# Kernel tuning notes

Measured on AMD Instinct MI355X. Metric: run time of the kernel, lower is better.

## Reference

```python
import jax, jax.numpy as jnp
import numpy as np

# loss weights / thresholds (match module defaults)
L_RC, L_HU, L_EDGE, L_TEX = 2.0, 1.5, 1.0, 0.8
L_HF, L_SYN, L_IC, L_MID, L_LF = 1.5, 1.0, 0.8, 0.8, 0.6
MIN_BODY, ART_FACTOR, FLAT_TH = 4096, 2.0, 0.03

SOBEL_X = jnp.array([[-1., 0., 1.], [-2., 0., 2.], [-1., 0., 1.]], jnp.float32)
SOBEL_Y = jnp.array([[-1., -2., -1.], [0., 0., 0.], [1., 2., 1.]], jnp.float32)
LAP = jnp.array([[0., 1., 0.], [1., -4., 1.], [0., 1., 0.]], jnp.float32)

def _conv2d(x, k):
    # x: (B,1,H,W), k: (kh,kw), 'same' padding single-channel conv
    kh, kw = k.shape
    return jax.lax.conv_general_dilated(
        x, k[None, None].astype(x.dtype), (1, 1),
        [(kh // 2, kh // 2), (kw // 2, kw // 2)],
        dimension_numbers=('NCHW', 'OIHW', 'NCHW'))

def _gauss_kernel(sigma):
    k = int(6 * sigma + 1)
    if k % 2 == 0:
        k += 1
    c = jnp.arange(k, dtype=jnp.float32) - k // 2
    g = jnp.exp(-0.5 * (c / sigma) ** 2)
    g = g / g.sum()
    return g[:, None] * g[None, :]

def _masked_mean(x, mask):
    cnt = jnp.sum(mask)
    return jnp.sum(jnp.where(mask, x, 0.0)) / jnp.maximum(cnt, 1)

def _masked_l1(a, b, mask):
    cnt = jnp.sum(mask)
    return jnp.sum(jnp.where(mask, jnp.abs(a - b), 0.0)) / jnp.maximum(cnt, 1)

def _masked_quantile(x, mask, q):
    # torch.quantile(x[mask], q) with linear interpolation
    v = jnp.sort(jnp.where(mask, x, jnp.inf).ravel())
    n = jnp.maximum(jnp.sum(mask), 1)
    pos = q * (n - 1).astype(x.dtype)
    lo = jnp.clip(jnp.floor(pos).astype(jnp.int32), 0, v.size - 1)
    hi = jnp.clip(jnp.ceil(pos).astype(jnp.int32), 0, v.size - 1)
    frac = pos - lo.astype(x.dtype)
    return v[lo] * (1.0 - frac) + v[hi] * frac

def setup_inputs() -> dict:
    key = jax.random.key(0)
    ks = jax.random.split(key, 7)
    B, H, W = 16, 768, 768
    return {
        'y_pred': jax.random.uniform(ks[0], (B, 1, 1, H, W), jnp.float32),
        'noise_pred': jax.random.normal(ks[1], (B, 1, 1, H, W), jnp.float32),
        'x_i': jax.random.uniform(ks[2], (B, 1, H, W), jnp.float32),
        'x_ip1': jax.random.uniform(ks[3], (B, 1, H, W), jnp.float32),
        'x_mid': jax.random.uniform(ks[4], (B, 1, H, W), jnp.float32),
        'W': jax.random.uniform(ks[5], (B, 1, H, W), jnp.float32),
        'noise_synthetic': jax.random.normal(ks[6], (B, 1, H, W), jnp.float32),
    }

def reference(y_pred, noise_pred, x_i, x_ip1, x_mid, W, noise_synthetic):
    yp = y_pred[:, :, 0]          # (B,1,H,W)
    npred = noise_pred[:, :, 0]

    # reconstruction
    loss_rc = jnp.mean(jnp.abs(yp * W - x_i * W))

    # HU consistency on body mask
    body = (x_i > 0.15) & (x_i < 0.85)
    nb = jnp.sum(body)
    mean_in = _masked_mean(x_i, body)
    mean_pr = _masked_mean(yp, body)
    hu = (mean_pr - mean_in) ** 2 + 0.5 * (
        (_masked_quantile(yp, body, 0.25) - _masked_quantile(x_i, body, 0.25)) ** 2
        + (_masked_quantile(yp, body, 0.75) - _masked_quantile(x_i, body, 0.75)) ** 2)
    loss_hu = jnp.where(nb > MIN_BODY, hu, 0.0)

    # edges
    gxp, gyp = _conv2d(yp, SOBEL_X), _conv2d(yp, SOBEL_Y)
    gxi, gyi = _conv2d(x_i, SOBEL_X), _conv2d(x_i, SOBEL_Y)
    loss_edge = jnp.mean(jnp.abs(gxp - gxi)) + jnp.mean(jnp.abs(gyp - gyi))

    gmi = jnp.sqrt(gxi ** 2 + gyi ** 2 + 1e-8)
    gmp = jnp.sqrt(gxp ** 2 + gyp ** 2 + 1e-8)

    # texture
    tex = (gmi > FLAT_TH) & (gmi < 0.5)
    loss_texture = jnp.where(jnp.sum(tex) > 100, _masked_l1(gmp, gmi, tex), 0.0)

    flat = gmi < FLAT_TH
    fb = flat & body
    nfb = jnp.sum(fb)

    # low/mid frequency losses on flat body regions
    G3, G1 = _gauss_kernel(3.0), _gauss_kernel(1.0)
    low_i, low_p, low_m = _conv2d(x_i, G3), _conv2d(yp, G3), _conv2d(x_mid, G3)
    lf = _masked_l1(low_p - low_m, 0.3 * (low_i - low_m), fb)
    mid_i = _conv2d(x_i, G1) - low_i
    mid_p = _conv2d(yp, G1) - low_p
    mid = _masked_l1(jnp.abs(mid_p), 0.3 * jnp.abs(mid_i), fb)
    loss_lf = jnp.where(nfb > 100, lf, 0.0)
    loss_mid = jnp.where(nfb > 100, mid, 0.0)

    # high-frequency noise via laplacian on flat regions
    lap_i, lap_p = _conv2d(x_i, LAP), _conv2d(yp, LAP)
    nf = jnp.sum(flat)
    loss_hf = jnp.where(nf > 100, _masked_l1(jnp.abs(lap_p), 0.3 * jnp.abs(lap_i), flat), 0.0)

    # synthetic noise supervision on flat body
    loss_syn = jnp.where(nfb > 100, _masked_l1(npred, noise_synthetic, fb), 0.0)

    # artifact penalty on flat regions
    ic = _masked_mean(jnp.maximum(gmp - ART_FACTOR * gmi, 0.0), flat)
    loss_ic = jnp.where(nf > 100, ic, 0.0)

    total = (L_RC * loss_rc + L_HU * loss_hu + L_EDGE * loss_edge
             + L_TEX * loss_texture + L_HF * loss_hf + L_MID * loss_mid
             + L_LF * loss_lf + L_SYN * loss_syn + L_IC * loss_ic)
    return total
```

## Files before the change

### kernel.cpp

```cpp
#include <hip/hip_runtime.h>


#define HH 768
#define WW 768
#define BB 16
#define HWSZ (HH * WW)
#define NPXD ((double)BB * (double)HWSZ)

#define NB 1024
#define NHIST (2 * NB)
#define NCOPY 8

#define STRIPS 3
#define HSEG 6
#define NSEG (HH / HSEG)
#define NJOBS (STRIPS * NSEG * BB)
#define NBLK1 (NJOBS / 4)

#define FBBUF 128

__device__ __forceinline__ float wredf(float v) {
#pragma unroll
  for (int o = 32; o > 0; o >>= 1) v += __shfl_down(v, o, 64);
  return v;
}
__device__ __forceinline__ unsigned wredu(unsigned v) {
#pragma unroll
  for (int o = 32; o > 0; o >>= 1) v += __shfl_down(v, o, 64);
  return v;
}

struct Row {
  float f[4];
  float l, r;
};

__device__ __forceinline__ Row load_row(const float* __restrict__ p, int y,
                                        int xl, int x0, int lane) {
  Row r;
  if (y < 0 || y >= HH) {
    r.f[0] = r.f[1] = r.f[2] = r.f[3] = 0.f;
    r.l = 0.f;
    r.r = 0.f;
    return r;
  }
  const float4 v = *(const float4*)(p + (size_t)y * WW + xl);
  r.f[0] = v.x; r.f[1] = v.y; r.f[2] = v.z; r.f[3] = v.w;
  float left = __shfl_up(v.w, 1, 64);
  float right = __shfl_down(v.x, 1, 64);
  if (lane == 0) left = (x0 > 0) ? p[(size_t)y * WW + x0 - 1] : 0.f;
  if (lane == 63) right = (x0 + 256 < WW) ? p[(size_t)y * WW + x0 + 256] : 0.f;
  r.l = left;
  r.r = right;
  return r;
}

#define LNB(row, j) ((j) == 0 ? (row).l : (row).f[(j)-1])
#define RNB(row, j) ((j) == 3 ? (row).r : (row).f[(j) + 1])


__global__ __launch_bounds__(256) void pass1_kernel(
    const float* __restrict__ yp, const float* __restrict__ xi,
    const float* __restrict__ wt, double* __restrict__ accs,
    unsigned* __restrict__ cnts, unsigned* __restrict__ fb_list, int fb_cap,
    unsigned* __restrict__ hist_final) {
  __shared__ unsigned s_hist[NHIST];
  __shared__ unsigned s_fb[4][FBBUF];
  __shared__ unsigned s_fbn[4];
  __shared__ float s_redf[4][8];
  __shared__ unsigned s_redc[4][3];

  const int tid = threadIdx.x;
  const int lane = tid & 63;
  const int wv = tid >> 6;
  const unsigned long long lmask_lt = (1ull << lane) - 1ull;

  for (int i = tid; i < NHIST; i += 256) s_hist[i] = 0u;
  if (lane == 0) s_fbn[wv] = 0u;
  __syncthreads();

  const int job = blockIdx.x * 4 + wv;
  const int s = job % STRIPS;
  const int seg = (job / STRIPS) % NSEG;
  const int b = job / (STRIPS * NSEG);
  const int x0 = s * 256;
  const int y0 = seg * HSEG;
  const int xl = x0 + lane * 4;
  const size_t base = (size_t)b * HWSZ;
  const float* ypb = yp + base;
  const float* xib = xi + base;
  const float* wtb = wt + base;

  float a_rc = 0.f, a_sxi = 0.f, a_syp = 0.f, a_ex = 0.f, a_ey = 0.f;
  float a_tex = 0.f, a_hf = 0.f, a_ic = 0.f;
  unsigned c_body = 0u, c_tex = 0u, c_flat = 0u;

  Row pm1 = load_row(ypb, y0 - 1, xl, x0, lane);
  Row pc = load_row(ypb, y0, xl, x0, lane);
  Row im1 = load_row(xib, y0 - 1, xl, x0, lane);
  Row icr = load_row(xib, y0, xl, x0, lane);

  for (int y = y0; y < y0 + HSEG; y++) {
    const Row pp1 = load_row(ypb, y + 1, xl, x0, lane);
    const Row ip1 = load_row(xib, y + 1, xl, x0, lane);
    const float4 w4 = *(const float4*)(wtb + (size_t)y * WW + xl);
    const float wf[4] = {w4.x, w4.y, w4.z, w4.w};

#pragma unroll
    for (int j = 0; j < 4; j++) {
      const float p00 = LNB(pm1, j), p01 = pm1.f[j], p02 = RNB(pm1, j);
      const float p10 = LNB(pc, j),  p11 = pc.f[j],  p12 = RNB(pc, j);
      const float p20 = LNB(pp1, j), p21 = pp1.f[j], p22 = RNB(pp1, j);
      const float i00 = LNB(im1, j), i01 = im1.f[j], i02 = RNB(im1, j);
      const float i10 = LNB(icr, j), i11 = icr.f[j], i12 = RNB(icr, j);
      const float i20 = LNB(ip1, j), i21 = ip1.f[j], i22 = RNB(ip1, j);

      const float gxp = (p02 - p00) + 2.f * (p12 - p10) + (p22 - p20);
      const float gyp = (p20 - p00) + 2.f * (p21 - p01) + (p22 - p02);
      const float lapp = p01 + p10 + p12 + p21 - 4.f * p11;
      const float gxi_ = (i02 - i00) + 2.f * (i12 - i10) + (i22 - i20);
      const float gyi_ = (i20 - i00) + 2.f * (i21 - i01) + (i22 - i02);
      const float lapi = i01 + i10 + i12 + i21 - 4.f * i11;

      const float yv = p11, xv = i11;
      a_rc += fabsf(yv * wf[j] - xv * wf[j]);

      const bool body = (xv > 0.15f) && (xv < 0.85f);
      if (body) {
        c_body++;
        a_sxi += xv;
        a_syp += yv;
        int bx = (int)(xv * (float)NB);
        bx = bx < 0 ? 0 : (bx > NB - 1 ? NB - 1 : bx);
        int by = (int)(yv * (float)NB);
        by = by < 0 ? 0 : (by > NB - 1 ? NB - 1 : by);
        atomicAdd(&s_hist[bx], 1u);
        atomicAdd(&s_hist[NB + by], 1u);
      }

      a_ex += fabsf(gxp - gxi_);
      a_ey += fabsf(gyp - gyi_);

      const float gmi = sqrtf(gxi_ * gxi_ + gyi_ * gyi_ + 1e-8f);
      const float gmp = sqrtf(gxp * gxp + gyp * gyp + 1e-8f);

      if (gmi > 0.03f && gmi < 0.5f) {
        c_tex++;
        a_tex += fabsf(gmp - gmi);
      }
      const bool flat = gmi < 0.03f;
      if (flat) {
        c_flat++;
        a_hf += fabsf(fabsf(lapp) - 0.3f * fabsf(lapi));
        a_ic += fmaxf(gmp - 2.0f * gmi, 0.f);
      }
      const bool qual = flat && body;
      const unsigned long long m = __ballot(qual);
      if (m) {
        const unsigned bofs = s_fbn[wv];
        if (qual) {
          const unsigned p = bofs + (unsigned)__popcll(m & lmask_lt);
          const unsigned gidx = (unsigned)(base + (size_t)y * WW + (xl + j));
          if (p < FBBUF) {
            s_fb[wv][p] = gidx;
          } else {
            const unsigned gi = atomicAdd(&cnts[3], 1u);
            if ((int)gi < fb_cap) fb_list[gi] = gidx;
          }
        }
        s_fbn[wv] = bofs + (unsigned)__popcll(m);
      }
    }
    pm1 = pc; pc = pp1;
    im1 = icr; icr = ip1;
  }

  {
    unsigned n = s_fbn[wv];
    if (n > FBBUF) n = FBBUF;
    unsigned gbase = 0u;
    if (lane == 0 && n > 0) gbase = atomicAdd(&cnts[3], n);
    gbase = __shfl(gbase, 0, 64);
    for (unsigned i = lane; i < n; i += 64) {
      const unsigned gi = gbase + i;
      if ((int)gi < fb_cap) fb_list[gi] = s_fb[wv][i];
    }
  }

  __syncthreads();
  {
    const unsigned hco = ((unsigned)blockIdx.x & (NCOPY - 1)) * NHIST;
    for (int i = tid; i < NHIST; i += 256) {
      const unsigned v = s_hist[i];
      if (v) atomicAdd(&hist_final[hco + i], v);
    }
  }

  float f0 = wredf(a_rc), f1 = wredf(a_sxi), f2 = wredf(a_syp);
  float f3 = wredf(a_ex), f4 = wredf(a_ey), f5 = wredf(a_tex);
  float f6 = wredf(a_hf), f7 = wredf(a_ic);
  unsigned u0 = wredu(c_body), u1 = wredu(c_tex), u2 = wredu(c_flat);
  if (lane == 0) {
    s_redf[wv][0] = f0; s_redf[wv][1] = f1; s_redf[wv][2] = f2; s_redf[wv][3] = f3;
    s_redf[wv][4] = f4; s_redf[wv][5] = f5; s_redf[wv][6] = f6; s_redf[wv][7] = f7;
    s_redc[wv][0] = u0; s_redc[wv][1] = u1; s_redc[wv][2] = u2;
  }
  __syncthreads();
  if (tid < 8) {
    double sm = (double)s_redf[0][tid] + (double)s_redf[1][tid] +
                (double)s_redf[2][tid] + (double)s_redf[3][tid];
    atomicAdd(&accs[tid], sm);
  } else if (tid < 11) {
    int k = tid - 8;
    unsigned sm = s_redc[0][k] + s_redc[1][k] + s_redc[2][k] + s_redc[3][k];
    atomicAdd(&cnts[k], sm);
  }
}

__global__ __launch_bounds__(256) void pass2_kernel(
    const float* __restrict__ yp, const float* __restrict__ xi,
    const float* __restrict__ xm, const float* __restrict__ npred,
    const float* __restrict__ nsyn, double* __restrict__ accs,
    const unsigned* __restrict__ cnts, const unsigned* __restrict__ fb_list,
    int fb_cap) {
  __shared__ float w3[19];
  __shared__ float w1[7];
  __shared__ double s_red[4][3];
  const int tid = threadIdx.x;
  const int lane = tid & 63;
  const int wv = tid >> 6;

  if (tid == 0) {
    float tmp[19], s = 0.f;
    for (int i = 0; i < 19; i++) {
      float c = (float)(i - 9) / 3.0f;
      tmp[i] = expf(-0.5f * c * c);
      s += tmp[i];
    }
    for (int i = 0; i < 19; i++) w3[i] = tmp[i] / s;
    float tmp1[7], s1 = 0.f;
    for (int i = 0; i < 7; i++) {
      float c = (float)(i - 3);
      tmp1[i] = expf(-0.5f * c * c);
      s1 += tmp1[i];
    }
    for (int i = 0; i < 7; i++) w1[i] = tmp1[i] / s1;
  }
  __syncthreads();

  unsigned nfb = cnts[3];
  if (nfb > (unsigned)fb_cap) nfb = (unsigned)fb_cap;
  const int wid = (int)((blockIdx.x * blockDim.x + tid) >> 6);
  const int nwaves = (int)((gridDim.x * blockDim.x) >> 6);

  double w_lf = 0.0, w_md = 0.0, w_sy = 0.0;

  for (int i = wid; i < (int)nfb; i += nwaves) {
    const unsigned px = fb_list[i];
    const int b = (int)(px / (unsigned)HWSZ);
    const int rem = (int)(px % (unsigned)HWSZ);
    const int y = rem / WW;
    const int x = rem % WW;
    const size_t base = (size_t)b * HWSZ;
    const float* xib = xi + base;
    const float* ypb = yp + base;
    const float* xmb = xm + base;

    float npv = 0.f, nsv = 0.f;
    if (lane == 0) { npv = npred[px]; nsv = nsyn[px]; }

    float s_li = 0.f, s_lp = 0.f, s_lm = 0.f;
    float s_gi = 0.f, s_gp = 0.f;
    const bool interior = (y >= 9) && (y < HH - 9) && (x >= 9) && (x < WW - 9);
    if (interior) {
#pragma unroll
      for (int k = 0; k < 6; k++) {
        const int tap = lane + 64 * k;
        if (tap < 361) {
          const int r = tap / 19, c = tap - r * 19;
          const float wgt = w3[r] * w3[c];
          const int o = (y + r - 9) * WW + (x + c - 9);
          s_li += wgt * xib[o];
          s_lp += wgt * ypb[o];
          s_lm += wgt * xmb[o];
        }
      }
      if (lane < 49) {
        const int r = lane / 7, c = lane - r * 7;
        const float wgt = w1[r] * w1[c];
        const int o = (y + r - 3) * WW + (x + c - 3);
        s_gi = wgt * xib[o];
        s_gp = wgt * ypb[o];
      }
    } else {
#pragma unroll
      for (int k = 0; k < 6; k++) {
        const int tap = lane + 64 * k;
        if (tap < 361) {
          const int r = tap / 19, c = tap - r * 19;
          const int gy = y + r - 9, gx = x + c - 9;
          if (gy >= 0 && gy < HH && gx >= 0 && gx < WW) {
            const float wgt = w3[r] * w3[c];
            const int o = gy * WW + gx;
            s_li += wgt * xib[o];
            s_lp += wgt * ypb[o];
            s_lm += wgt * xmb[o];
          }
        }
      }
      if (lane < 49) {
        const int r = lane / 7, c = lane - r * 7;
        const int gy = y + r - 3, gx = x + c - 3;
        if (gy >= 0 && gy < HH && gx >= 0 && gx < WW) {
          const float wgt = w1[r] * w1[c];
          const int o = gy * WW + gx;
          s_gi = wgt * xib[o];
          s_gp = wgt * ypb[o];
        }
      }
    }
    s_li = wredf(s_li);
    s_lp = wredf(s_lp);
    s_lm = wredf(s_lm);
    s_gi = wredf(s_gi);
    s_gp = wredf(s_gp);
    if (lane == 0) {
      const float lf = fabsf((s_lp - s_lm) - 0.3f * (s_li - s_lm));
      const float mi_ = s_gi - s_li, mp_ = s_gp - s_lp;
      const float md = fabsf(fabsf(mp_) - 0.3f * fabsf(mi_));
      w_lf += (double)lf;
      w_md += (double)md;
      w_sy += (double)fabsf(npv - nsv);
    }
  }

  if (lane == 0) {
    s_red[wv][0] = w_lf; s_red[wv][1] = w_md; s_red[wv][2] = w_sy;
  }
  __syncthreads();
  if (tid < 3) {
    const double t = s_red[0][tid] + s_red[1][tid] + s_red[2][tid] + s_red[3][tid];
    if (t != 0.0) atomicAdd(&accs[8 + tid], t);
  }
}

__global__ __launch_bounds__(256) void finalize_kernel(
    const double* __restrict__ accs, const unsigned* __restrict__ cnts,
    const unsigned* __restrict__ hist, float* __restrict__ out) {
  __shared__ unsigned sc[NHIST];
  __shared__ unsigned wsum[8];
  __shared__ double quant[4];
  const int tid = threadIdx.x;
  const int lane = tid & 63;
  const int wv = tid >> 6;

  if (tid < 4) quant[tid] = 0.0;

#pragma unroll
  for (int h = 0; h < 2; h++) {
    const int baseh = h * NB + tid * 4;
    unsigned v0 = 0u, v1 = 0u, v2 = 0u, v3 = 0u;
#pragma unroll
    for (int c = 0; c < NCOPY; c++) {
      const unsigned* hb = hist + c * NHIST + baseh;
      v0 += hb[0];
      v1 += hb[1];
      v2 += hb[2];
      v3 += hb[3];
    }
    const unsigned s = v0 + v1 + v2 + v3;
    unsigned scl = s;
#pragma unroll
    for (int o = 1; o < 64; o <<= 1) {
      const unsigned t = __shfl_up(scl, o, 64);
      if (lane >= o) scl += t;
    }
    if (lane == 63) wsum[h * 4 + wv] = scl;
    __syncthreads();
    unsigned woff = 0;
    for (int k = 0; k < wv; k++) woff += wsum[h * 4 + k];
    const unsigned excl = woff + scl - s;
    const unsigned c0 = excl + v0;
    const unsigned c1 = c0 + v1;
    const unsigned c2 = c1 + v2;
    const unsigned c3 = c2 + v3;
    sc[baseh + 0] = c0;
    sc[baseh + 1] = c1;
    sc[baseh + 2] = c2;
    sc[baseh + 3] = c3;
    __syncthreads();
  }

  const unsigned nb = cnts[0];
  if (tid < 4 && nb > 4096u) {
    const int h = tid >> 1;
    const double q = (tid & 1) ? 0.75 : 0.25;
    const double pos = q * (double)(nb - 1u);
    int lo = 0, hi = NB - 1;
    while (lo < hi) {
      const int mid = (lo + hi) >> 1;
      if ((double)sc[h * NB + mid] > pos) hi = mid; else lo = mid + 1;
    }
    const unsigned cum_before = (lo > 0) ? sc[h * NB + lo - 1] : 0u;
    const unsigned m = sc[h * NB + lo] - cum_before;
    const double local = pos - (double)cum_before;
    quant[tid] = ((double)lo + (local + 0.5) / (double)(m ? m : 1u)) *
                 (1.0 / (double)NB);
  }
  __syncthreads();
  if (tid != 0) return;

  const unsigned ntex = cnts[1], nflat = cnts[2], nfb = cnts[3];
  const double loss_rc = accs[0] / NPXD;
  const double denb = (double)(nb > 0u ? nb : 1u);
  const double mean_in = accs[1] / denb;
  const double mean_pr = accs[2] / denb;

  double loss_hu = 0.0;
  if (nb > 4096u) {
    const double q25i = quant[0], q75i = quant[1];
    const double q25p = quant[2], q75p = quant[3];
    const double d = mean_pr - mean_in;
    loss_hu = d * d + 0.5 * ((q25p - q25i) * (q25p - q25i) +
                             (q75p - q75i) * (q75p - q75i));
  }

  const double loss_edge = accs[3] / NPXD + accs[4] / NPXD;
  const double loss_tex = (ntex > 100u) ? accs[5] / (double)(ntex ? ntex : 1u) : 0.0;
  const double loss_hf = (nflat > 100u) ? accs[6] / (double)(nflat ? nflat : 1u) : 0.0;
  const double loss_ic = (nflat > 100u) ? accs[7] / (double)(nflat ? nflat : 1u) : 0.0;
  const double denfb = (double)(nfb > 0u ? nfb : 1u);
  const double loss_lf = (nfb > 100u) ? accs[8] / denfb : 0.0;
  const double loss_mid = (nfb > 100u) ? accs[9] / denfb : 0.0;
  const double loss_syn = (nfb > 100u) ? accs[10] / denfb : 0.0;

  const double total = 2.0 * loss_rc + 1.5 * loss_hu + 1.0 * loss_edge +
                       0.8 * loss_tex + 1.5 * loss_hf + 0.8 * loss_mid +
                       0.6 * loss_lf + 1.0 * loss_syn + 0.8 * loss_ic;
  out[0] = (float)total;
}

extern "C" void kernel_launch(void* const* d_in, const int* in_sizes, int n_in,
                              void* d_out, int out_size, void* d_ws,
                              size_t ws_size, hipStream_t stream) {
  (void)in_sizes; (void)n_in; (void)out_size;
  const float* y_pred = (const float*)d_in[0];
  const float* noise_pred = (const float*)d_in[1];
  const float* x_i = (const float*)d_in[2];
  const float* x_mid = (const float*)d_in[4];
  const float* Wt = (const float*)d_in[5];
  const float* nsyn = (const float*)d_in[6];
  float* out = (float*)d_out;

  char* ws = (char*)d_ws;
  double* accs = (double*)ws;
  unsigned* cnts = (unsigned*)(ws + 128);
  unsigned* hist_final = (unsigned*)(ws + 256);
  const size_t FIXED = 256 + (size_t)NCOPY * NHIST * 4;

  size_t avail = (ws_size > FIXED) ? (ws_size - FIXED) : 0;
  long long cap = (long long)(avail / 4);
  if (cap > (long long)BB * HWSZ) cap = (long long)BB * HWSZ;
  int fb_cap = (int)cap;
  unsigned* fb_list = (unsigned*)(ws + FIXED);

  hipMemsetAsync(ws, 0, FIXED, stream);
  pass1_kernel<<<NBLK1, 256, 0, stream>>>(y_pred, x_i, Wt, accs, cnts,
                                          fb_list, fb_cap, hist_final);
  pass2_kernel<<<512, 256, 0, stream>>>(y_pred, x_i, x_mid, noise_pred, nsyn,
                                        accs, cnts, fb_list, fb_cap);
  finalize_kernel<<<1, 256, 0, stream>>>(accs, cnts, hist_final, out);
}
```

Measured before the change: 269.1 us.

## Software-pipeline row loads two rows ahead and double segment height

Splits row loading into an issue step and a finish step so global loads for rows two ahead are in flight while the current row is computed, and fully unrolls the per-segment loop. Segment height doubles, halving the number of jobs and the redundant halo row loads per job. The shared-memory fb-list counter becomes a register. This adds register pressure and cuts the number of blocks, which may reduce occupancy and latency hiding.

```diff
diff --git a/kernel.cpp b/kernel.cpp
--- a/kernel.cpp
+++ b/kernel.cpp
@@ -12,7 +12,7 @@
 #define NCOPY 8
 
 #define STRIPS 3
-#define HSEG 6
+#define HSEG 12
 #define NSEG (HH / HSEG)
 #define NJOBS (STRIPS * NSEG * BB)
 #define NBLK1 (NJOBS / 4)
@@ -35,21 +35,37 @@
   float l, r;
 };
 
-__device__ __forceinline__ Row load_row(const float* __restrict__ p, int y,
-                                        int xl, int x0, int lane) {
+struct RawRow {
+  float4 v;
+  float eL, eR;
+};
+
+__device__ __forceinline__ RawRow issue_row(const float* __restrict__ p,
+                                            int y, int xl, int x0, int lane) {
+  RawRow r;
+  const float* rp = p + (size_t)y * WW;
+  r.v = *(const float4*)(rp + xl);
+  r.eL = 0.f;
+  r.eR = 0.f;
+  if (lane == 0 && x0 > 0) r.eL = rp[x0 - 1];
+  if (lane == 63 && x0 + 256 < WW) r.eR = rp[x0 + 256];
+  return r;
+}
+
+__device__ __forceinline__ Row finish_row(const RawRow& rr, bool valid,
+                                          int lane) {
   Row r;
-  if (y < 0 || y >= HH) {
+  if (!valid) {
     r.f[0] = r.f[1] = r.f[2] = r.f[3] = 0.f;
     r.l = 0.f;
     r.r = 0.f;
     return r;
   }
-  const float4 v = *(const float4*)(p + (size_t)y * WW + xl);
-  r.f[0] = v.x; r.f[1] = v.y; r.f[2] = v.z; r.f[3] = v.w;
-  float left = __shfl_up(v.w, 1, 64);
-  float right = __shfl_down(v.x, 1, 64);
-  if (lane == 0) left = (x0 > 0) ? p[(size_t)y * WW + x0 - 1] : 0.f;
-  if (lane == 63) right = (x0 + 256 < WW) ? p[(size_t)y * WW + x0 + 256] : 0.f;
+  r.f[0] = rr.v.x; r.f[1] = rr.v.y; r.f[2] = rr.v.z; r.f[3] = rr.v.w;
+  float left = __shfl_up(rr.v.w, 1, 64);
+  float right = __shfl_down(rr.v.x, 1, 64);
+  if (lane == 0) left = rr.eL;
+  if (lane == 63) right = rr.eR;
   r.l = left;
   r.r = right;
   return r;
@@ -66,7 +82,6 @@
     unsigned* __restrict__ hist_final) {
   __shared__ unsigned s_hist[NHIST];
   __shared__ unsigned s_fb[4][FBBUF];
-  __shared__ unsigned s_fbn[4];
   __shared__ float s_redf[4][8];
   __shared__ unsigned s_redc[4][3];
 
@@ -76,14 +91,13 @@
   const unsigned long long lmask_lt = (1ull << lane) - 1ull;
 
   for (int i = tid; i < NHIST; i += 256) s_hist[i] = 0u;
-  if (lane == 0) s_fbn[wv] = 0u;
   __syncthreads();
 
   const int job = blockIdx.x * 4 + wv;
-  const int s = job % STRIPS;
+  const int st = job % STRIPS;
   const int seg = (job / STRIPS) % NSEG;
   const int b = job / (STRIPS * NSEG);
-  const int x0 = s * 256;
+  const int x0 = st * 256;
   const int y0 = seg * HSEG;
   const int xl = x0 + lane * 4;
   const size_t base = (size_t)b * HWSZ;
@@ -94,16 +108,49 @@
   float a_rc = 0.f, a_sxi = 0.f, a_syp = 0.f, a_ex = 0.f, a_ey = 0.f;
   float a_tex = 0.f, a_hf = 0.f, a_ic = 0.f;
   unsigned c_body = 0u, c_tex = 0u, c_flat = 0u;
-
-  Row pm1 = load_row(ypb, y0 - 1, xl, x0, lane);
-  Row pc = load_row(ypb, y0, xl, x0, lane);
-  Row im1 = load_row(xib, y0 - 1, xl, x0, lane);
-  Row icr = load_row(xib, y0, xl, x0, lane);
-
-  for (int y = y0; y < y0 + HSEG; y++) {
-    const Row pp1 = load_row(ypb, y + 1, xl, x0, lane);
-    const Row ip1 = load_row(xib, y + 1, xl, x0, lane);
-    const float4 w4 = *(const float4*)(wtb + (size_t)y * WW + xl);
+  unsigned fbn = 0u;
+
+  const int ym1 = (y0 > 0) ? y0 - 1 : 0;
+  RawRow t0 = issue_row(ypb, ym1, xl, x0, lane);
+  RawRow t1 = issue_row(ypb, y0, xl, x0, lane);
+  RawRow t2 = issue_row(xib, ym1, xl, x0, lane);
+  RawRow t3 = issue_row(xib, y0, xl, x0, lane);
+
+  RawRow pA[2], iA[2];
+  float4 wA[2];
+  pA[0] = issue_row(ypb, y0 + 1, xl, x0, lane);
+  iA[0] = issue_row(xib, y0 + 1, xl, x0, lane);
+  wA[0] = *(const float4*)(wtb + (size_t)y0 * WW + xl);
+  pA[1] = issue_row(ypb, y0 + 2, xl, x0, lane);
+  iA[1] = issue_row(xib, y0 + 2, xl, x0, lane);
+  wA[1] = *(const float4*)(wtb + (size_t)(y0 + 1) * WW + xl);
+
+  Row pm1 = finish_row(t0, y0 > 0, lane);
+  Row pc  = finish_row(t1, true, lane);
+  Row im1 = finish_row(t2, y0 > 0, lane);
+  Row icr = finish_row(t3, true, lane);
+
+#pragma unroll
+  for (int k = 0; k < HSEG; k++) {
+    const int y = y0 + k;
+    const int s2 = k & 1;
+
+    RawRow np = {};
+    RawRow ni = {};
+    float4 nw = {};
+    if (k + 3 <= HSEG) {
+      const int r = y + 3;
+      const int rc = (r < HH) ? r : HH - 1;
+      np = issue_row(ypb, rc, xl, x0, lane);
+      ni = issue_row(xib, rc, xl, x0, lane);
+    }
+    if (k + 2 <= HSEG - 1) {
+      nw = *(const float4*)(wtb + (size_t)(y + 2) * WW + xl);
+    }
+
+    const Row pp1 = finish_row(pA[s2], y + 1 < HH, lane);
+    const Row ip1 = finish_row(iA[s2], y + 1 < HH, lane);
+    const float4 w4 = wA[s2];
     const float wf[4] = {w4.x, w4.y, w4.z, w4.w};
 
 #pragma unroll
@@ -157,9 +204,8 @@
       const bool qual = flat && body;
       const unsigned long long m = __ballot(qual);
       if (m) {
-        const unsigned bofs = s_fbn[wv];
         if (qual) {
-          const unsigned p = bofs + (unsigned)__popcll(m & lmask_lt);
+          const unsigned p = fbn + (unsigned)__popcll(m & lmask_lt);
           const unsigned gidx = (unsigned)(base + (size_t)y * WW + (xl + j));
           if (p < FBBUF) {
             s_fb[wv][p] = gidx;
@@ -168,15 +214,18 @@
             if ((int)gi < fb_cap) fb_list[gi] = gidx;
           }
         }
-        s_fbn[wv] = bofs + (unsigned)__popcll(m);
-      }
-    }
+        fbn += (unsigned)__popcll(m);
+      }
+    }
+
+    if (k + 3 <= HSEG) { pA[s2] = np; iA[s2] = ni; }
+    if (k + 2 <= HSEG - 1) wA[s2] = nw;
     pm1 = pc; pc = pp1;
     im1 = icr; icr = ip1;
   }
 
   {
-    unsigned n = s_fbn[wv];
+    unsigned n = fbn;
     if (n > FBBUF) n = FBBUF;
     unsigned gbase = 0u;
     if (lane == 0 && n > 0) gbase = atomicAdd(&cnts[3], n);
```

New measurement: 276.6 us. 2.8% more time.

## Process full-width rows per wavefront with software-pipelined row prefetch

Applied to the files above, without the earlier changes.

Each wavefront now covers a full 768-pixel row (12 pixels per lane, three float4 loads) instead of 256-pixel strips. This removes the per-lane halo scalar loads at strip edges and the redundant overlapping column reads. Loads for the next row are issued before computing the current one in a double-buffered even/odd scheme. Block indices are swizzled across groups of eight, and the shared-memory fb counter becomes a register. The cost is much higher register pressure from 12-wide rows across six neighbor rows plus prefetch buffers, which may lower occupancy.

```diff
diff --git a/kernel.cpp b/kernel.cpp
--- a/kernel.cpp
+++ b/kernel.cpp
@@ -11,13 +11,12 @@
 #define NHIST (2 * NB)
 #define NCOPY 8
 
-#define STRIPS 3
 #define HSEG 6
 #define NSEG (HH / HSEG)
-#define NJOBS (STRIPS * NSEG * BB)
+#define NJOBS (BB * NSEG)
 #define NBLK1 (NJOBS / 4)
 
-#define FBBUF 128
+#define FBBUF 192
 
 __device__ __forceinline__ float wredf(float v) {
 #pragma unroll
@@ -30,34 +29,129 @@
   return v;
 }
 
-struct Row {
-  float f[4];
+struct RawF {
+  float4 a, b, c;
+};
+
+__device__ __forceinline__ RawF issue_frow(const float* __restrict__ p, int y,
+                                           int lane) {
+  const float* rp = p + (size_t)y * WW + lane * 12;
+  RawF r;
+  r.a = *(const float4*)(rp);
+  r.b = *(const float4*)(rp + 4);
+  r.c = *(const float4*)(rp + 8);
+  return r;
+}
+
+struct FRow {
+  float f[12];
   float l, r;
 };
 
-__device__ __forceinline__ Row load_row(const float* __restrict__ p, int y,
-                                        int xl, int x0, int lane) {
-  Row r;
-  if (y < 0 || y >= HH) {
-    r.f[0] = r.f[1] = r.f[2] = r.f[3] = 0.f;
+__device__ __forceinline__ FRow finish_frow(const RawF& rr, bool valid,
+                                            int lane) {
+  FRow r;
+  if (!valid) {
+#pragma unroll
+    for (int i = 0; i < 12; i++) r.f[i] = 0.f;
     r.l = 0.f;
     r.r = 0.f;
     return r;
   }
-  const float4 v = *(const float4*)(p + (size_t)y * WW + xl);
-  r.f[0] = v.x; r.f[1] = v.y; r.f[2] = v.z; r.f[3] = v.w;
-  float left = __shfl_up(v.w, 1, 64);
-  float right = __shfl_down(v.x, 1, 64);
-  if (lane == 0) left = (x0 > 0) ? p[(size_t)y * WW + x0 - 1] : 0.f;
-  if (lane == 63) right = (x0 + 256 < WW) ? p[(size_t)y * WW + x0 + 256] : 0.f;
-  r.l = left;
-  r.r = right;
+  r.f[0] = rr.a.x; r.f[1] = rr.a.y; r.f[2] = rr.a.z; r.f[3] = rr.a.w;
+  r.f[4] = rr.b.x; r.f[5] = rr.b.y; r.f[6] = rr.b.z; r.f[7] = rr.b.w;
+  r.f[8] = rr.c.x; r.f[9] = rr.c.y; r.f[10] = rr.c.z; r.f[11] = rr.c.w;
+  const float lf = __shfl_up(rr.c.w, 1, 64);
+  const float rt = __shfl_down(rr.a.x, 1, 64);
+  r.l = (lane == 0) ? 0.f : lf;
+  r.r = (lane == 63) ? 0.f : rt;
   return r;
 }
 
 #define LNB(row, j) ((j) == 0 ? (row).l : (row).f[(j)-1])
-#define RNB(row, j) ((j) == 3 ? (row).r : (row).f[(j) + 1])
-
+#define RNB(row, j) ((j) == 11 ? (row).r : (row).f[(j) + 1])
+#define RF(r, j)                                                            \
+  ((j) == 0 ? (r).a.x : (j) == 1 ? (r).a.y : (j) == 2 ? (r).a.z :           \
+   (j) == 3 ? (r).a.w : (j) == 4 ? (r).b.x : (j) == 5 ? (r).b.y :           \
+   (j) == 6 ? (r).b.z : (j) == 7 ? (r).b.w : (j) == 8 ? (r).c.x :           \
+   (j) == 9 ? (r).c.y : (j) == 10 ? (r).c.z : (r).c.w)
+
+
+__device__ __forceinline__ void row_body(
+    const FRow& pm1, const FRow& pc, const FRow& pp1, const FRow& im1,
+    const FRow& icr, const FRow& ip1, const RawF& wr, int y, size_t base,
+    int lane, unsigned long long lmask_lt, float& a_rc, float& a_sxi,
+    float& a_syp, float& a_ex, float& a_ey, float& a_tex, float& a_hf,
+    float& a_ic, unsigned& c_body, unsigned& c_tex, unsigned& c_flat,
+    unsigned& fbn, unsigned* s_hist, unsigned* s_fbw,
+    unsigned* __restrict__ cnts, unsigned* __restrict__ fb_list, int fb_cap) {
+  const int xg0 = lane * 12;
+#pragma unroll
+  for (int j = 0; j < 12; j++) {
+    const float p00 = LNB(pm1, j), p01 = pm1.f[j], p02 = RNB(pm1, j);
+    const float p10 = LNB(pc, j),  p11 = pc.f[j],  p12 = RNB(pc, j);
+    const float p20 = LNB(pp1, j), p21 = pp1.f[j], p22 = RNB(pp1, j);
+    const float i00 = LNB(im1, j), i01 = im1.f[j], i02 = RNB(im1, j);
+    const float i10 = LNB(icr, j), i11 = icr.f[j], i12 = RNB(icr, j);
+    const float i20 = LNB(ip1, j), i21 = ip1.f[j], i22 = RNB(ip1, j);
+
+    const float gxp = (p02 - p00) + 2.f * (p12 - p10) + (p22 - p20);
+    const float gyp = (p20 - p00) + 2.f * (p21 - p01) + (p22 - p02);
+    const float lapp = p01 + p10 + p12 + p21 - 4.f * p11;
+    const float gxi_ = (i02 - i00) + 2.f * (i12 - i10) + (i22 - i20);
+    const float gyi_ = (i20 - i00) + 2.f * (i21 - i01) + (i22 - i02);
+    const float lapi = i01 + i10 + i12 + i21 - 4.f * i11;
+
+    const float yv = p11, xv = i11;
+    const float wfj = RF(wr, j);
+    a_rc += fabsf(yv * wfj - xv * wfj);
+
+    const bool body = (xv > 0.15f) && (xv < 0.85f);
+    if (body) {
+      c_body++;
+      a_sxi += xv;
+      a_syp += yv;
+      int bx = (int)(xv * (float)NB);
+      bx = bx < 0 ? 0 : (bx > NB - 1 ? NB - 1 : bx);
+      int by = (int)(yv * (float)NB);
+      by = by < 0 ? 0 : (by > NB - 1 ? NB - 1 : by);
+      atomicAdd(&s_hist[bx], 1u);
+      atomicAdd(&s_hist[NB + by], 1u);
+    }
+
+    a_ex += fabsf(gxp - gxi_);
+    a_ey += fabsf(gyp - gyi_);
+
+    const float gmi = sqrtf(gxi_ * gxi_ + gyi_ * gyi_ + 1e-8f);
+    const float gmp = sqrtf(gxp * gxp + gyp * gyp + 1e-8f);
+
+    if (gmi > 0.03f && gmi < 0.5f) {
+      c_tex++;
+      a_tex += fabsf(gmp - gmi);
+    }
+    const bool flat = gmi < 0.03f;
+    if (flat) {
+      c_flat++;
+      a_hf += fabsf(fabsf(lapp) - 0.3f * fabsf(lapi));
+      a_ic += fmaxf(gmp - 2.0f * gmi, 0.f);
+    }
+    const bool qual = flat && body;
+    const unsigned long long m = __ballot(qual);
+    if (m) {
+      if (qual) {
+        const unsigned p = fbn + (unsigned)__popcll(m & lmask_lt);
+        const unsigned gidx = (unsigned)(base + (size_t)y * WW + (xg0 + j));
+        if (p < FBBUF) {
+          s_fbw[p] = gidx;
+        } else {
+          const unsigned gi = atomicAdd(&cnts[3], 1u);
+          if ((int)gi < fb_cap) fb_list[gi] = gidx;
+        }
+      }
+      fbn += (unsigned)__popcll(m);
+    }
+  }
+}
 
 __global__ __launch_bounds__(256) void pass1_kernel(
     const float* __restrict__ yp, const float* __restrict__ xi,
@@ -66,7 +160,6 @@
     unsigned* __restrict__ hist_final) {
   __shared__ unsigned s_hist[NHIST];
   __shared__ unsigned s_fb[4][FBBUF];
-  __shared__ unsigned s_fbn[4];
   __shared__ float s_redf[4][8];
   __shared__ unsigned s_redc[4][3];
 
@@ -76,16 +169,13 @@
   const unsigned long long lmask_lt = (1ull << lane) - 1ull;
 
   for (int i = tid; i < NHIST; i += 256) s_hist[i] = 0u;
-  if (lane == 0) s_fbn[wv] = 0u;
   __syncthreads();
 
-  const int job = blockIdx.x * 4 + wv;
-  const int s = job % STRIPS;
-  const int seg = (job / STRIPS) % NSEG;
-  const int b = job / (STRIPS * NSEG);
-  const int x0 = s * 256;
+  const int sb = ((int)blockIdx.x & 7) * (NBLK1 / 8) + ((int)blockIdx.x >> 3);
+  const int job = sb * 4 + wv;
+  const int seg = job & (NSEG - 1);
+  const int b = job / NSEG;
   const int y0 = seg * HSEG;
-  const int xl = x0 + lane * 4;
   const size_t base = (size_t)b * HWSZ;
   const float* ypb = yp + base;
   const float* xib = xi + base;
@@ -94,96 +184,66 @@
   float a_rc = 0.f, a_sxi = 0.f, a_syp = 0.f, a_ex = 0.f, a_ey = 0.f;
   float a_tex = 0.f, a_hf = 0.f, a_ic = 0.f;
   unsigned c_body = 0u, c_tex = 0u, c_flat = 0u;
-
-  Row pm1 = load_row(ypb, y0 - 1, xl, x0, lane);
-  Row pc = load_row(ypb, y0, xl, x0, lane);
-  Row im1 = load_row(xib, y0 - 1, xl, x0, lane);
-  Row icr = load_row(xib, y0, xl, x0, lane);
-
-  for (int y = y0; y < y0 + HSEG; y++) {
-    const Row pp1 = load_row(ypb, y + 1, xl, x0, lane);
-    const Row ip1 = load_row(xib, y + 1, xl, x0, lane);
-    const float4 w4 = *(const float4*)(wtb + (size_t)y * WW + xl);
-    const float wf[4] = {w4.x, w4.y, w4.z, w4.w};
-
-#pragma unroll
-    for (int j = 0; j < 4; j++) {
-      const float p00 = LNB(pm1, j), p01 = pm1.f[j], p02 = RNB(pm1, j);
-      const float p10 = LNB(pc, j),  p11 = pc.f[j],  p12 = RNB(pc, j);
-      const float p20 = LNB(pp1, j), p21 = pp1.f[j], p22 = RNB(pp1, j);
-      const float i00 = LNB(im1, j), i01 = im1.f[j], i02 = RNB(im1, j);
-      const float i10 = LNB(icr, j), i11 = icr.f[j], i12 = RNB(icr, j);
-      const float i20 = LNB(ip1, j), i21 = ip1.f[j], i22 = RNB(ip1, j);
-
-      const float gxp = (p02 - p00) + 2.f * (p12 - p10) + (p22 - p20);
-      const float gyp = (p20 - p00) + 2.f * (p21 - p01) + (p22 - p02);
-      const float lapp = p01 + p10 + p12 + p21 - 4.f * p11;
-      const float gxi_ = (i02 - i00) + 2.f * (i12 - i10) + (i22 - i20);
-      const float gyi_ = (i20 - i00) + 2.f * (i21 - i01) + (i22 - i02);
-      const float lapi = i01 + i10 + i12 + i21 - 4.f * i11;
-
-      const float yv = p11, xv = i11;
-      a_rc += fabsf(yv * wf[j] - xv * wf[j]);
-
-      const bool body = (xv > 0.15f) && (xv < 0.85f);
-      if (body) {
-        c_body++;
-        a_sxi += xv;
-        a_syp += yv;
-        int bx = (int)(xv * (float)NB);
-        bx = bx < 0 ? 0 : (bx > NB - 1 ? NB - 1 : bx);
-        int by = (int)(yv * (float)NB);
-        by = by < 0 ? 0 : (by > NB - 1 ? NB - 1 : by);
-        atomicAdd(&s_hist[bx], 1u);
-        atomicAdd(&s_hist[NB + by], 1u);
-      }
-
-      a_ex += fabsf(gxp - gxi_);
-      a_ey += fabsf(gyp - gyi_);
-
-      const float gmi = sqrtf(gxi_ * gxi_ + gyi_ * gyi_ + 1e-8f);
-      const float gmp = sqrtf(gxp * gxp + gyp * gyp + 1e-8f);
-
-      if (gmi > 0.03f && gmi < 0.5f) {
-        c_tex++;
-        a_tex += fabsf(gmp - gmi);
-      }
-      const bool flat = gmi < 0.03f;
-      if (flat) {
-        c_flat++;
-        a_hf += fabsf(fabsf(lapp) - 0.3f * fabsf(lapi));
-        a_ic += fmaxf(gmp - 2.0f * gmi, 0.f);
-      }
-      const bool qual = flat && body;
-      const unsigned long long m = __ballot(qual);
-      if (m) {
-        const unsigned bofs = s_fbn[wv];
-        if (qual) {
-          const unsigned p = bofs + (unsigned)__popcll(m & lmask_lt);
-          const unsigned gidx = (unsigned)(base + (size_t)y * WW + (xl + j));
-          if (p < FBBUF) {
-            s_fb[wv][p] = gidx;
-          } else {
-            const unsigned gi = atomicAdd(&cnts[3], 1u);
-            if ((int)gi < fb_cap) fb_list[gi] = gidx;
-          }
-        }
-        s_fbn[wv] = bofs + (unsigned)__popcll(m);
-      }
-    }
-    pm1 = pc; pc = pp1;
-    im1 = icr; icr = ip1;
+  unsigned fbn = 0u;
+  unsigned* s_fbw = s_fb[wv];
+
+  const int ym1 = (y0 > 0) ? y0 - 1 : 0;
+  RawF t0 = issue_frow(ypb, ym1, lane);
+  RawF t1 = issue_frow(ypb, y0, lane);
+  RawF t2 = issue_frow(xib, ym1, lane);
+  RawF t3 = issue_frow(xib, y0, lane);
+  RawF rpE = issue_frow(ypb, y0 + 1, lane);
+  RawF riE = issue_frow(xib, y0 + 1, lane);
+  RawF wE = issue_frow(wtb, y0, lane);
+
+  FRow pm1 = finish_frow(t0, y0 > 0, lane);
+  FRow pc = finish_frow(t1, true, lane);
+  FRow im1 = finish_frow(t2, y0 > 0, lane);
+  FRow icr = finish_frow(t3, true, lane);
+
+  RawF rpO, riO, wO;
+
+  for (int k = 0; k < HSEG; k += 2) {
+    {
+      const int y = y0 + k;
+      const int yi2 = (y + 2 < HH) ? y + 2 : HH - 1;
+      rpO = issue_frow(ypb, yi2, lane);
+      riO = issue_frow(xib, yi2, lane);
+      const int yw = (k + 1 < HSEG) ? y + 1 : y;
+      wO = issue_frow(wtb, yw, lane);
+      const FRow pp1 = finish_frow(rpE, true, lane);
+      const FRow ip1 = finish_frow(riE, true, lane);
+      row_body(pm1, pc, pp1, im1, icr, ip1, wE, y, base, lane, lmask_lt,
+               a_rc, a_sxi, a_syp, a_ex, a_ey, a_tex, a_hf, a_ic, c_body,
+               c_tex, c_flat, fbn, s_hist, s_fbw, cnts, fb_list, fb_cap);
+      pm1 = pc; pc = pp1; im1 = icr; icr = ip1;
+    }
+    {
+      const int y = y0 + k + 1;
+      const int yi2 = (y + 2 < HH) ? y + 2 : HH - 1;
+      rpE = issue_frow(ypb, yi2, lane);
+      riE = issue_frow(xib, yi2, lane);
+      const int yw = (k + 2 < HSEG) ? y + 1 : y;
+      wE = issue_frow(wtb, yw, lane);
+      const bool v = (y + 1 < HH);
+      const FRow pp1 = finish_frow(rpO, v, lane);
+      const FRow ip1 = finish_frow(riO, v, lane);
+      row_body(pm1, pc, pp1, im1, icr, ip1, wO, y, base, lane, lmask_lt,
+               a_rc, a_sxi, a_syp, a_ex, a_ey, a_tex, a_hf, a_ic, c_body,
+               c_tex, c_flat, fbn, s_hist, s_fbw, cnts, fb_list, fb_cap);
+      pm1 = pc; pc = pp1; im1 = icr; icr = ip1;
+    }
   }
 
   {
-    unsigned n = s_fbn[wv];
+    unsigned n = fbn;
     if (n > FBBUF) n = FBBUF;
     unsigned gbase = 0u;
     if (lane == 0 && n > 0) gbase = atomicAdd(&cnts[3], n);
     gbase = __shfl(gbase, 0, 64);
     for (unsigned i = lane; i < n; i += 64) {
       const unsigned gi = gbase + i;
-      if ((int)gi < fb_cap) fb_list[gi] = s_fb[wv][i];
+      if ((int)gi < fb_cap) fb_list[gi] = s_fbw[i];
     }
   }
 
```

After: 269.5 us. About the same (+0.1%).
